# Optimization experiments

Hardware: AMD Instinct MI355X
Metric: run time of the kernel (lower is better)

Reference implementation:

```python
import jax, jax.numpy as jnp
import numpy as np
import math

B, CIN, W = 8, 1, 1024
D, H, NL, NE, DFF = 256, 2, 2, 10, 1024
LAT = W // 2
DK = D // H

def _pe_table(max_len, d):
    pos = np.arange(max_len)[:, None].astype(np.float32)
    div = np.exp(np.arange(0, d, 2).astype(np.float32) * (-math.log(10000.0) / d))
    pe = np.zeros((max_len, d), np.float32)
    pe[:, 0::2] = np.sin(pos * div)
    pe[:, 1::2] = np.cos(pos * div)
    return jnp.asarray(pe[None])

def _ln(x, g, b, eps=1e-5):
    mu = jnp.mean(x, -1, keepdims=True)
    var = jnp.mean(jnp.square(x - mu), -1, keepdims=True)
    return (x - mu) * jax.lax.rsqrt(var + eps) * g + b

def setup_inputs() -> dict:
    key = jax.random.key(0)
    ks = iter(jax.random.split(key, 64))
    tn = lambda shape: 0.02 * jax.random.truncated_normal(next(ks), -2.0, 2.0, shape, jnp.float32)
    return dict(
        x=jax.random.normal(next(ks), (B, CIN, W), jnp.float32),
        conv_w=tn((D, CIN, 5)), conv_b=tn((D,)),
        pe=_pe_table(LAT, D),
        ln0_g=jnp.ones((D,), jnp.float32), ln0_b=jnp.zeros((D,), jnp.float32),
        wq=tn((NL, D, D)), bq=tn((NL, D)),
        wk=tn((NL, D, D)), bk=tn((NL, D)),
        wv=tn((NL, D, D)), bv=tn((NL, D)),
        wo=tn((NL, D, D)), bo=tn((NL, D)),
        ln1_g=jnp.ones((NL, D), jnp.float32), ln1_b=jnp.zeros((NL, D), jnp.float32),
        ln2_g=jnp.ones((NL, D), jnp.float32), ln2_b=jnp.zeros((NL, D), jnp.float32),
        router_w=tn((NL, NE, D)), router_b=tn((NL, NE)),
        e_w1=tn((NL, NE, D, DFF)), e_b1=tn((NL, NE, DFF)),
        e_w2=tn((NL, NE, DFF, D)), e_b2=tn((NL, NE, D)),
        deconv_w=tn((D, D, 4)), deconv_b=tn((D,)),
        lin1_w=tn((128, D)), lin1_b=tn((128,)),
        lin2_w=tn((1, 128)), lin2_b=tn((1,)),
    )

def _forward(x, conv_w, conv_b, pe, ln0_g, ln0_b, wq, bq, wk, bk, wv, bv, wo, bo,
             ln1_g, ln1_b, ln2_g, ln2_b, router_w, router_b,
             e_w1, e_b1, e_w2, e_b2, deconv_w, deconv_b,
             lin1_w, lin1_b, lin2_w, lin2_b):
    # Conv1d(k=5, p=2, replicate) tokenizer + LPPool1d(p=2, k=2, s=2)
    xp = jnp.pad(x, ((0, 0), (0, 0), (2, 2)), mode='edge')
    h = jax.lax.conv_general_dilated(xp, conv_w, window_strides=(1,), padding=[(0, 0)],
                                     dimension_numbers=('NCH', 'OIH', 'NCH'))
    h = h + conv_b[None, :, None]
    h = jnp.sqrt(jnp.sum(jnp.square(h).reshape(B, D, LAT, 2), -1))   # LP pool, p=2
    z = h.transpose(0, 2, 1) + pe                                     # [B, LAT, D]
    z = _ln(z, ln0_g, ln0_b)
    counts_l, rprob_l = [], []
    for l in range(NL):
        q = (z @ wq[l].T + bq[l]).reshape(B, LAT, H, DK).transpose(0, 2, 1, 3)
        k = (z @ wk[l].T + bk[l]).reshape(B, LAT, H, DK).transpose(0, 2, 1, 3)
        v = (z @ wv[l].T + bv[l]).reshape(B, LAT, H, DK).transpose(0, 2, 1, 3)
        attn = jax.nn.softmax(jnp.einsum('bhqd,bhkd->bhqk', q, k) / math.sqrt(DK), -1)
        a = jnp.einsum('bhqk,bhkd->bhqd', attn, v).transpose(0, 2, 1, 3).reshape(B, LAT, D)
        z = _ln(z + (a @ wo[l].T + bo[l]), ln1_g[l], ln1_b[l])
        # Switch FFN: top-1 routing, no token drop, scale output by max route prob
        t = z.reshape(-1, D)                                          # [T, D]
        rp = jax.nn.softmax(t @ router_w[l].T + router_b[l], -1)      # [T, E]
        routes = jnp.argmax(rp, -1)
        rmax = jnp.max(rp, -1)
        hh = jax.nn.relu(jnp.einsum('td,edf->tef', t, e_w1[l]) + e_b1[l])
        yy = jnp.einsum('tef,efd->ted', hh, e_w2[l]) + e_b2[l]
        y = yy[jnp.arange(t.shape[0]), routes] * rmax[:, None]
        counts_l.append(jnp.sum(jax.nn.one_hot(routes, NE, dtype=jnp.float32), 0))
        rprob_l.append(jnp.sum(rp, 0))
        z = _ln(z + y.reshape(B, LAT, D), ln2_g[l], ln2_b[l])
    # ConvTranspose1d(k=4, s=2, p=1) == dilated conv with flipped/transposed kernel
    dw = jnp.flip(deconv_w, -1).transpose(1, 0, 2)                    # [out, in, k]
    u = jax.lax.conv_general_dilated(z.transpose(0, 2, 1), dw, window_strides=(1,),
                                     padding=[(2, 2)], lhs_dilation=(2,),
                                     dimension_numbers=('NCH', 'OIH', 'NCH'))
    u = (u + deconv_b[None, :, None]).transpose(0, 2, 1)              # [B, W, D]
    u = jnp.tanh(u @ lin1_w.T + lin1_b)
    out = (u @ lin2_w.T + lin2_b).transpose(0, 2, 1)                  # [B, 1, W]
    counts = jnp.stack(counts_l)                                      # [NL, NE]
    rprob = jnp.stack(rprob_l)
    total = jnp.sum(counts, -1, keepdims=True)
    loss_moe = NE * jnp.sum((counts / total) * (rprob / total))
    return out, loss_moe

def reference(x, conv_w, conv_b, pe, ln0_g, ln0_b, wq, bq, wk, bk, wv, bv, wo, bo,
              ln1_g, ln1_b, ln2_g, ln2_b, router_w, router_b,
              e_w1, e_b1, e_w2, e_b2, deconv_w, deconv_b,
              lin1_w, lin1_b, lin2_w, lin2_b):
    return _forward(x, conv_w, conv_b, pe, ln0_g, ln0_b, wq, bq, wk, bk, wv, bv, wo, bo,
                    ln1_g, ln1_b, ln2_g, ln2_b, router_w, router_b,
                    e_w1, e_b1, e_w2, e_b2, deconv_w, deconv_b,
                    lin1_w, lin1_b, lin2_w, lin2_b)
```

## Files before the change

kernel.cpp:

```cpp
#include <hip/hip_runtime.h>
#include <math.h>

#define LATN 512
#define DN 256
#define DKN 128
#define TTOT 4096
#define NEXP 10
#define DFFN 1024

using bf16x8 = __attribute__((ext_vector_type(8))) short;
using f32x4  = __attribute__((ext_vector_type(4))) float;

__device__ __forceinline__ float dot4(float4 a, float4 b) {
    return a.x*b.x + a.y*b.y + a.z*b.z + a.w*b.w;
}

__device__ __forceinline__ unsigned short f2bf(float f) {
    union { float f; unsigned int u; } v; v.f = f;
    unsigned int u = v.u + 0x7FFFu + ((v.u >> 16) & 1u);
    return (unsigned short)(u >> 16);
}

__device__ __forceinline__ float block_reduce_sum(float v, float* red) {
    #pragma unroll
    for (int off = 32; off; off >>= 1) v += __shfl_down(v, off, 64);
    int lane = threadIdx.x & 63, wid = threadIdx.x >> 6;
    if (lane == 0) red[wid] = v;
    __syncthreads();
    float r = red[0] + red[1] + red[2] + red[3];
    __syncthreads();
    return r;
}

__device__ __forceinline__ float wave_sum(float x) {
    #pragma unroll
    for (int off = 32; off; off >>= 1) x += __shfl_xor(x, off, 64);
    return x;
}

__global__ void zero_kernel(float* rprob_p, int* ec_p) {
    int i = threadIdx.x;
    if (i < 320) { rprob_p[i] = 0.f; ec_p[i] = 0; }
}

__global__ void tokenizer_kernel(const float* __restrict__ x, const float* __restrict__ cw,
                                 const float* __restrict__ cb, const float* __restrict__ pe,
                                 const float* __restrict__ g, const float* __restrict__ bb,
                                 float* __restrict__ z) {
    int blk = blockIdx.x;
    int l = blk & (LATN - 1);
    int b = blk >> 9;
    int d = threadIdx.x;
    __shared__ float red[8];
    const float* xb = x + (size_t)b * 1024;
    float w0 = cw[d*5+0], w1 = cw[d*5+1], w2 = cw[d*5+2], w3 = cw[d*5+3], w4 = cw[d*5+4];
    float bv = cb[d];
    int p0 = 2 * l;
    auto xc = [&](int i) { return xb[min(max(i, 0), 1023)]; };
    float h0 = bv + w0*xc(p0-2) + w1*xc(p0-1) + w2*xc(p0)   + w3*xc(p0+1) + w4*xc(p0+2);
    float h1 = bv + w0*xc(p0-1) + w1*xc(p0)   + w2*xc(p0+1) + w3*xc(p0+2) + w4*xc(p0+3);
    float pool = sqrtf(h0*h0 + h1*h1);
    float val = pool + pe[l*DN + d];
    float s = block_reduce_sum(val, red);
    float mu = s * (1.0f/DN);
    float dv = val - mu;
    float s2 = block_reduce_sum(dv*dv, red);
    float r = rsqrtf(s2 * (1.0f/DN) + 1e-5f);
    z[((size_t)b*LATN + l)*DN + d] = dv*r*g[d] + bb[d];
}

__global__ void pack_proj(const float* __restrict__ wq, const float* __restrict__ wk,
                          const float* __restrict__ wv, const float* __restrict__ wo,
                          unsigned short* __restrict__ wp) {
    int mat = blockIdx.y;
    int l0 = mat >> 2, which = mat & 3;
    const float* base = (which == 0) ? wq : (which == 1) ? wk : (which == 2) ? wv : wo;
    const float* W = base + l0*65536;
    int tid = blockIdx.x*256 + threadIdx.x;
    int l = tid & 63, kk = (tid >> 6) & 7, nt = tid >> 9;
    const float* src = W + (size_t)(nt*16 + (l&15))*DN + kk*32 + (l>>4)*8;
    unsigned short o[8];
    #pragma unroll
    for (int j = 0; j < 8; ++j) o[j] = f2bf(src[j]);
    *(ulonglong2*)(wp + (size_t)mat*65536 + (size_t)tid*8) = *(ulonglong2*)o;
}

template<int OM>
__device__ __forceinline__ void proj_body(const float* __restrict__ A,
                                          const unsigned short* __restrict__ wpm,
                                          const float* __restrict__ bias,
                                          void* __restrict__ outp, int t0, float oscale,
                                          unsigned short* ts) {
    int tid = threadIdx.x;
    #pragma unroll
    for (int i = 0; i < 16; ++i) {
        int f4 = i*256 + tid;
        int row = f4 >> 6, c4 = f4 & 63;
        float4 a = *(const float4*)&A[(size_t)(t0+row)*DN + c4*4];
        ushort4 o = { f2bf(a.x), f2bf(a.y), f2bf(a.z), f2bf(a.w) };
        *(ushort4*)&ts[row*264 + c4*4] = o;
    }
    __syncthreads();
    int w = tid >> 6, l = tid & 63;
    f32x4 acc[4][4];
    #pragma unroll
    for (int m = 0; m < 4; ++m)
        #pragma unroll
        for (int n = 0; n < 4; ++n) acc[m][n] = (f32x4){0.f,0.f,0.f,0.f};
    const bf16x8* wv = (const bf16x8*)wpm;
    #pragma unroll
    for (int kk = 0; kk < 8; ++kk) {
        bf16x8 af[4];
        #pragma unroll
        for (int m = 0; m < 4; ++m)
            af[m] = *(const bf16x8*)&ts[(m*16 + (l&15))*264 + kk*32 + (l>>4)*8];
        #pragma unroll
        for (int n = 0; n < 4; ++n) {
            bf16x8 bf = wv[((w*4 + n)*8 + kk)*64 + l];
            #pragma unroll
            for (int m = 0; m < 4; ++m)
                acc[m][n] = __builtin_amdgcn_mfma_f32_16x16x32_bf16(af[m], bf, acc[m][n], 0, 0, 0);
        }
    }
    #pragma unroll
    for (int n = 0; n < 4; ++n) {
        int col = w*64 + n*16 + (l&15);
        float bv2 = bias[col];
        #pragma unroll
        for (int m = 0; m < 4; ++m) {
            #pragma unroll
            for (int r = 0; r < 4; ++r) {
                int row = t0 + m*16 + (l>>4)*4 + r;
                float val = acc[m][n][r] + bv2;
                if (OM == 0)
                    ((float*)outp)[(size_t)row*DN + col] = val;
                else if (OM == 1)
                    ((unsigned short*)outp)[(size_t)row*DN + col] = f2bf(val * oscale);
                else
                    ((unsigned short*)outp)[(((size_t)(row>>9)*2 + (col>>7))*128 + (col&127))*512 + (row&511)] = f2bf(val);
            }
        }
    }
}

__global__ __launch_bounds__(256)
void proj_qkv(const float* __restrict__ z, const unsigned short* __restrict__ wp,
              const float* __restrict__ bq, const float* __restrict__ bk,
              const float* __restrict__ bv,
              unsigned short* __restrict__ qb, unsigned short* __restrict__ kb,
              unsigned short* __restrict__ vtb) {
    __shared__ unsigned short ts[64*264];
    int mat = blockIdx.y;
    if (mat == 0)      proj_body<1>(z, wp,          bq, qb,  blockIdx.x*64, 0.08838834764831844f, ts);
    else if (mat == 1) proj_body<1>(z, wp + 65536,  bk, kb,  blockIdx.x*64, 1.0f, ts);
    else               proj_body<2>(z, wp + 131072, bv, vtb, blockIdx.x*64, 1.0f, ts);
}

__global__ __launch_bounds__(256)
void proj_one(const float* __restrict__ A, const unsigned short* __restrict__ wpm,
              const float* __restrict__ bias, float* __restrict__ out) {
    __shared__ unsigned short ts[64*264];
    proj_body<0>(A, wpm, bias, out, blockIdx.x*64, 1.0f, ts);
}

__global__ __launch_bounds__(256)
void attn_mfma(const unsigned short* __restrict__ qb, const unsigned short* __restrict__ kb,
               const unsigned short* __restrict__ vtb, float* __restrict__ a) {
    int blk = blockIdx.x;
    int xcd = blk & 7, idx = blk >> 3;
    int bh = xcd*2 + (idx & 1);
    int qt = idx >> 1;
    int b = bh >> 1, h = bh & 1;
    int q0 = qt * 32;
    int tid = threadIdx.x;
    int w = tid >> 6, l = tid & 63;
    int c = l & 15, g = l >> 4;

    __shared__ __align__(16) unsigned short p_lds[32*512];
    __shared__ float smax[4][2][16];
    __shared__ float ssum[4][2][16];

    bf16x8 qf_[2][4];
    #pragma unroll
    for (int qf = 0; qf < 2; ++qf)
        #pragma unroll
        for (int kk = 0; kk < 4; ++kk)
            qf_[qf][kk] = *(const bf16x8*)&qb[((size_t)(b*LATN + q0 + qf*16 + c))*DN + h*DKN + kk*32 + g*8];

    f32x4 st[8][2];
    #pragma unroll
    for (int f = 0; f < 8; ++f) { st[f][0] = (f32x4){0,0,0,0}; st[f][1] = (f32x4){0,0,0,0}; }
    #pragma unroll
    for (int f = 0; f < 8; ++f) {
        int kbase = w*128 + f*16;
        bf16x8 kf[4];
        #pragma unroll
        for (int kk = 0; kk < 4; ++kk)
            kf[kk] = *(const bf16x8*)&kb[((size_t)(b*LATN + kbase + c))*DN + h*DKN + kk*32 + g*8];
        #pragma unroll
        for (int kk = 0; kk < 4; ++kk) {
            st[f][0] = __builtin_amdgcn_mfma_f32_16x16x32_bf16(kf[kk], qf_[0][kk], st[f][0], 0, 0, 0);
            st[f][1] = __builtin_amdgcn_mfma_f32_16x16x32_bf16(kf[kk], qf_[1][kk], st[f][1], 0, 0, 0);
        }
    }

    float gmax[2], ginv[2];
    #pragma unroll
    for (int qf = 0; qf < 2; ++qf) {
        float m = -1e30f;
        #pragma unroll
        for (int f = 0; f < 8; ++f)
            #pragma unroll
            for (int r = 0; r < 4; ++r) m = fmaxf(m, st[f][qf][r]);
        m = fmaxf(m, __shfl_xor(m, 16, 64));
        m = fmaxf(m, __shfl_xor(m, 32, 64));
        if (l < 16) smax[w][qf][l] = m;
    }
    __syncthreads();
    #pragma unroll
    for (int qf = 0; qf < 2; ++qf)
        gmax[qf] = fmaxf(fmaxf(smax[0][qf][c], smax[1][qf][c]),
                         fmaxf(smax[2][qf][c], smax[3][qf][c]));
    #pragma unroll
    for (int qf = 0; qf < 2; ++qf) {
        float s = 0.f;
        #pragma unroll
        for (int f = 0; f < 8; ++f)
            #pragma unroll
            for (int r = 0; r < 4; ++r) {
                float e = __expf(st[f][qf][r] - gmax[qf]);
                st[f][qf][r] = e; s += e;
            }
        s += __shfl_xor(s, 16, 64);
        s += __shfl_xor(s, 32, 64);
        if (l < 16) ssum[w][qf][l] = s;
    }
    __syncthreads();
    #pragma unroll
    for (int qf = 0; qf < 2; ++qf)
        ginv[qf] = 1.0f / (ssum[0][qf][c] + ssum[1][qf][c] + ssum[2][qf][c] + ssum[3][qf][c]);

    #pragma unroll
    for (int qf = 0; qf < 2; ++qf) {
        int q_ = qf*16 + c;
        int rowb = q_ * 1024;
        int swz = (q_ & 7) << 4;
        float iv = ginv[qf];
        #pragma unroll
        for (int f = 0; f < 8; ++f) {
            unsigned int lo = (unsigned int)f2bf(st[f][qf][0]*iv) |
                              ((unsigned int)f2bf(st[f][qf][1]*iv) << 16);
            unsigned int hi = (unsigned int)f2bf(st[f][qf][2]*iv) |
                              ((unsigned int)f2bf(st[f][qf][3]*iv) << 16);
            int key0 = w*128 + f*16 + g*4;
            *(unsigned long long*)((char*)p_lds + rowb + ((key0*2) ^ swz)) =
                (unsigned long long)lo | ((unsigned long long)hi << 32);
        }
    }
    __syncthreads();

    f32x4 o[2][2];
    o[0][0] = (f32x4){0,0,0,0}; o[0][1] = (f32x4){0,0,0,0};
    o[1][0] = (f32x4){0,0,0,0}; o[1][1] = (f32x4){0,0,0,0};
    #pragma unroll
    for (int kk = 0; kk < 16; ++kk) {
        bf16x8 pb[2];
        #pragma unroll
        for (int qf = 0; qf < 2; ++qf) {
            int q_ = qf*16 + c;
            pb[qf] = *(const bf16x8*)((const char*)p_lds + q_*1024 +
                                      (((kk*32 + g*8)*2) ^ ((q_&7)<<4)));
        }
        bf16x8 va[2];
        #pragma unroll
        for (int m = 0; m < 2; ++m)
            va[m] = *(const bf16x8*)&vtb[((size_t)(bh*128 + w*32 + m*16 + c))*512 + kk*32 + g*8];
        #pragma unroll
        for (int m = 0; m < 2; ++m) {
            o[m][0] = __builtin_amdgcn_mfma_f32_16x16x32_bf16(va[m], pb[0], o[m][0], 0, 0, 0);
            o[m][1] = __builtin_amdgcn_mfma_f32_16x16x32_bf16(va[m], pb[1], o[m][1], 0, 0, 0);
        }
    }
    #pragma unroll
    for (int m = 0; m < 2; ++m)
        #pragma unroll
        for (int qf = 0; qf < 2; ++qf)
            #pragma unroll
            for (int r = 0; r < 4; ++r) {
                int d = w*32 + m*16 + g*4 + r;
                a[((size_t)(b*LATN + q0 + qf*16 + c))*DN + h*DKN + d] = o[m][qf][r];
            }
}

__global__ void ln_residual(float* __restrict__ z, const float* __restrict__ y,
                            const float* __restrict__ g, const float* __restrict__ b) {
    int t = blockIdx.x, tid = threadIdx.x;
    __shared__ float red[8];
    float val = z[(size_t)t*DN + tid] + y[(size_t)t*DN + tid];
    float s = block_reduce_sum(val, red);
    float mu = s * (1.0f/DN);
    float dv = val - mu;
    float s2 = block_reduce_sum(dv*dv, red);
    float r = rsqrtf(s2 * (1.0f/DN) + 1e-5f);
    z[(size_t)t*DN + tid] = dv*r*g[tid] + b[tid];
}

#define RTOK 32
__global__ __launch_bounds__(512)
void router_kernel(const float* __restrict__ z, const float* __restrict__ rw,
                   const float* __restrict__ rb, float* __restrict__ rmaxv,
                   float* __restrict__ rprob_p, int* __restrict__ ec_p,
                   int* __restrict__ elist) {
    __shared__ float rws[NEXP*DN];
    __shared__ float sprob[NEXP];
    __shared__ int lcnt[NEXP], lbase[NEXP];
    __shared__ int lrank[RTOK];
    __shared__ int lam[RTOK];
    int tid = threadIdx.x;
    for (int i = tid; i < NEXP*DN; i += 512) rws[i] = rw[i];
    if (tid < NEXP) { sprob[tid] = 0.f; lcnt[tid] = 0; }
    __syncthreads();
    int g = tid >> 4, j = tid & 15;
    int t = blockIdx.x * RTOK + g;
    const float4* z4 = (const float4*)&z[(size_t)t*DN + j*16];
    const float4* rws4 = (const float4*)rws;
    float acc[NEXP];
    #pragma unroll
    for (int e = 0; e < NEXP; ++e) acc[e] = 0.f;
    int r0 = (j >> 1) & 3;
    #pragma unroll
    for (int kq = 0; kq < 4; ++kq) {
        int k4 = (kq + r0) & 3;
        float4 zv = z4[k4];
        #pragma unroll
        for (int e = 0; e < NEXP; ++e)
            acc[e] += dot4(zv, rws4[e*64 + j*4 + k4]);
    }
    #pragma unroll
    for (int e = 0; e < NEXP; ++e) {
        acc[e] += __shfl_xor(acc[e], 1, 64);
        acc[e] += __shfl_xor(acc[e], 2, 64);
        acc[e] += __shfl_xor(acc[e], 4, 64);
        acc[e] += __shfl_xor(acc[e], 8, 64);
    }
    if (j == 0) {
        float lg[NEXP];
        float m = acc[0] + rb[0]; int am = 0;
        lg[0] = m;
        #pragma unroll
        for (int e = 1; e < NEXP; ++e) {
            lg[e] = acc[e] + rb[e];
            if (lg[e] > m) { m = lg[e]; am = e; }
        }
        float p[NEXP], s = 0.f;
        #pragma unroll
        for (int e = 0; e < NEXP; ++e) { p[e] = expf(lg[e] - m); s += p[e]; }
        float inv = 1.0f / s;
        rmaxv[t] = p[am] * inv;
        lam[g] = am;
        lrank[g] = atomicAdd(&lcnt[am], 1);
        #pragma unroll
        for (int e = 0; e < NEXP; ++e) atomicAdd(&sprob[e], p[e] * inv);
    }
    __syncthreads();
    if (tid < NEXP) {
        lbase[tid] = atomicAdd(&ec_p[tid*16], lcnt[tid]);
        atomicAdd(&rprob_p[tid*16], sprob[tid]);
    }
    __syncthreads();
    if (j == 0)
        elist[lam[g]*TTOT + lbase[lam[g]] + lrank[g]] = t;
}

__global__ void pack_w1(const float* __restrict__ w1l, unsigned short* __restrict__ w1p) {
    int tid = blockIdx.x*256 + threadIdx.x;
    int l = tid & 63, kk = (tid >> 6) & 7, nt = (tid >> 9) & 63, e = tid >> 15;
    const float* src = w1l + (size_t)e*262144 + (size_t)(kk*32 + (l>>4)*8)*DFFN + nt*16 + (l&15);
    unsigned short o[8];
    #pragma unroll
    for (int j = 0; j < 8; ++j) o[j] = f2bf(src[(size_t)j*DFFN]);
    ulonglong2* dst = (ulonglong2*)(w1p + (size_t)tid*8);
    *dst = *(ulonglong2*)o;
}

__global__ void pack_w2(const float* __restrict__ w2l, unsigned short* __restrict__ w2p) {
    int tid = blockIdx.x*256 + threadIdx.x;
    int l = tid & 63, kk = (tid >> 6) & 31, nt = (tid >> 11) & 15, e = tid >> 15;
    const float* src = w2l + (size_t)e*262144 + (size_t)(kk*32 + (l>>4)*8)*DN + nt*16 + (l&15);
    unsigned short o[8];
    #pragma unroll
    for (int j = 0; j < 8; ++j) o[j] = f2bf(src[(size_t)j*DN]);
    ulonglong2* dst = (ulonglong2*)(w2p + (size_t)tid*8);
    *dst = *(ulonglong2*)o;
}

#define TM 16
__global__ __launch_bounds__(256)
void moe_kernel(float* __restrict__ z, const int* __restrict__ elist,
                const int* __restrict__ ec_p, const float* __restrict__ rmaxv,
                const unsigned short* __restrict__ w1p, const float* __restrict__ b1,
                const unsigned short* __restrict__ w2p, const float* __restrict__ b2,
                const float* __restrict__ g, const float* __restrict__ bb) {
    int e = blockIdx.y;
    int cnt = ec_p[e*16];
    int base = blockIdx.x * TM;
    if (base >= cnt) return;
    int n = min(TM, cnt - base);

    __shared__ __align__(16) unsigned short ts[16*264];
    __shared__ __align__(16) unsigned short hbuf[16*1032];
    __shared__ __align__(16) float ybuf[16*260];
    __shared__ int toks[16];
    __shared__ float rm[16];

    int tid = threadIdx.x;
    int w = tid >> 6, l = tid & 63;
    if (tid < 16) {
        int tt = (tid < n) ? elist[e*TTOT + base + tid] : 0;
        toks[tid] = tt;
        rm[tid] = rmaxv[tt];
    }
    __syncthreads();
    #pragma unroll
    for (int m = 0; m < 16; ++m)
        ts[m*264 + tid] = f2bf(z[(size_t)toks[m]*DN + tid]);
    __syncthreads();

    const bf16x8* w1v = (const bf16x8*)w1p;
    const float* b1e = b1 + e*DFFN;
    f32x4 acc[16];
    #pragma unroll
    for (int i = 0; i < 16; ++i) acc[i] = (f32x4){0.f,0.f,0.f,0.f};
    #pragma unroll
    for (int kk = 0; kk < 8; ++kk) {
        bf16x8 a = *(const bf16x8*)(ts + (l&15)*264 + kk*32 + (l>>4)*8);
        const bf16x8* wbp = w1v + (((size_t)e*64 + w*16)*8 + kk)*64 + l;
        #pragma unroll
        for (int nt2 = 0; nt2 < 16; ++nt2)
            acc[nt2] = __builtin_amdgcn_mfma_f32_16x16x32_bf16(a, wbp[nt2*512], acc[nt2], 0, 0, 0);
    }
    #pragma unroll
    for (int nt2 = 0; nt2 < 16; ++nt2) {
        int col = w*256 + nt2*16 + (l&15);
        float bv = b1e[col];
        #pragma unroll
        for (int r = 0; r < 4; ++r) {
            int row = (l>>4)*4 + r;
            hbuf[row*1032 + col] = f2bf(fmaxf(acc[nt2][r] + bv, 0.f));
        }
    }
    __syncthreads();

    const bf16x8* w2v = (const bf16x8*)w2p;
    const float* b2e = b2 + e*DN;
    f32x4 acc2[4];
    #pragma unroll
    for (int i = 0; i < 4; ++i) acc2[i] = (f32x4){0.f,0.f,0.f,0.f};
    for (int kk = 0; kk < 32; ++kk) {
        bf16x8 a = *(const bf16x8*)(hbuf + (l&15)*1032 + kk*32 + (l>>4)*8);
        const bf16x8* wbp = w2v + (((size_t)e*16 + w*4)*32 + kk)*64 + l;
        #pragma unroll
        for (int nt2 = 0; nt2 < 4; ++nt2)
            acc2[nt2] = __builtin_amdgcn_mfma_f32_16x16x32_bf16(a, wbp[nt2*2048], acc2[nt2], 0, 0, 0);
    }
    #pragma unroll
    for (int nt2 = 0; nt2 < 4; ++nt2) {
        int col = w*64 + nt2*16 + (l&15);
        float bv = b2e[col];
        #pragma unroll
        for (int r = 0; r < 4; ++r) {
            int row = (l>>4)*4 + r;
            ybuf[row*260 + col] = (acc2[nt2][r] + bv) * rm[row];
        }
    }
    __syncthreads();

    #pragma unroll
    for (int rr = 0; rr < 4; ++rr) {
        int row = w*4 + rr;
        if (row < n) {
            int t = toks[row];
            float v[4];
            #pragma unroll
            for (int c = 0; c < 4; ++c)
                v[c] = ybuf[row*260 + l + 64*c] + z[(size_t)t*DN + l + 64*c];
            float s = wave_sum(v[0]+v[1]+v[2]+v[3]);
            float mu = s * (1.0f/DN);
            float s2 = 0.f;
            #pragma unroll
            for (int c = 0; c < 4; ++c) { v[c] -= mu; s2 += v[c]*v[c]; }
            s2 = wave_sum(s2);
            float rs = rsqrtf(s2 * (1.0f/DN) + 1e-5f);
            #pragma unroll
            for (int c = 0; c < 4; ++c) {
                int col = l + 64*c;
                z[(size_t)t*DN + col] = v[c]*rs*g[col] + bb[col];
            }
        }
    }
}

__global__ void pack_deconv_mfma(const float* __restrict__ w, unsigned short* __restrict__ wdp) {
    int tid = blockIdx.x*256 + threadIdx.x;
    int l = tid & 63, kk = (tid >> 6) & 7, nt = (tid >> 9) & 15, tap = tid >> 13;
    int dout = nt*16 + (l&15);
    int din0 = kk*32 + (l>>4)*8;
    unsigned short o[8];
    #pragma unroll
    for (int j = 0; j < 8; ++j)
        o[j] = f2bf(w[((size_t)(din0 + j)*DN + dout)*4 + tap]);
    *(ulonglong2*)(wdp + (size_t)tid*8) = *(ulonglong2*)o;
}

__global__ void pack_lin1(const float* __restrict__ w, unsigned short* __restrict__ wl1) {
    int tid = blockIdx.x*256 + threadIdx.x;
    int l = tid & 63, kk = (tid >> 6) & 7, nt = tid >> 9;
    const float* src = w + (size_t)(nt*16 + (l&15))*DN + kk*32 + (l>>4)*8;
    unsigned short o[8];
    #pragma unroll
    for (int j = 0; j < 8; ++j) o[j] = f2bf(src[j]);
    *(ulonglong2*)(wl1 + (size_t)tid*8) = *(ulonglong2*)o;
}

__global__ __launch_bounds__(256)
void deconv_mfma(const float* __restrict__ z, const unsigned short* __restrict__ wdp,
                 const float* __restrict__ db, float* __restrict__ u) {
    int blk = blockIdx.x;
    int b = blk >> 4, lt = blk & 15;
    int l0 = lt * 32;
    __shared__ __align__(16) unsigned short zs[34*264];
    int tid = threadIdx.x;
    #pragma unroll
    for (int i = 0; i < 9; ++i) {
        int f4 = i*256 + tid;
        if (f4 < 34*64) {
            int row = f4 >> 6, c4 = f4 & 63;
            int l = l0 - 1 + row;
            float4 a = (l >= 0 && l < LATN)
                ? *(const float4*)&z[((size_t)b*LATN + l)*DN + c4*4]
                : make_float4(0.f, 0.f, 0.f, 0.f);
            ushort4 o = { f2bf(a.x), f2bf(a.y), f2bf(a.z), f2bf(a.w) };
            *(ushort4*)&zs[row*264 + c4*4] = o;
        }
    }
    __syncthreads();
    int w = tid >> 6, l = tid & 63;
    f32x4 acce[2][4], acco[2][4];
    #pragma unroll
    for (int m = 0; m < 2; ++m)
        #pragma unroll
        for (int n = 0; n < 4; ++n) {
            acce[m][n] = (f32x4){0.f,0.f,0.f,0.f};
            acco[m][n] = (f32x4){0.f,0.f,0.f,0.f};
        }
    const bf16x8* wdv = (const bf16x8*)wdp;
    #pragma unroll
    for (int kk = 0; kk < 8; ++kk) {
        bf16x8 a0[2], a1[2], a2[2];
        #pragma unroll
        for (int m = 0; m < 2; ++m) {
            int rb = (m*16 + (l&15))*264 + kk*32 + (l>>4)*8;
            a0[m] = *(const bf16x8*)&zs[rb];
            a1[m] = *(const bf16x8*)&zs[rb + 264];
            a2[m] = *(const bf16x8*)&zs[rb + 528];
        }
        #pragma unroll
        for (int n = 0; n < 4; ++n) {
            int nt = w*4 + n;
            bf16x8 bt0 = wdv[((0*16 + nt)*8 + kk)*64 + l];
            bf16x8 bt1 = wdv[((1*16 + nt)*8 + kk)*64 + l];
            bf16x8 bt2 = wdv[((2*16 + nt)*8 + kk)*64 + l];
            bf16x8 bt3 = wdv[((3*16 + nt)*8 + kk)*64 + l];
            #pragma unroll
            for (int m = 0; m < 2; ++m) {
                acco[m][n] = __builtin_amdgcn_mfma_f32_16x16x32_bf16(a2[m], bt0, acco[m][n], 0, 0, 0);
                acce[m][n] = __builtin_amdgcn_mfma_f32_16x16x32_bf16(a1[m], bt1, acce[m][n], 0, 0, 0);
                acco[m][n] = __builtin_amdgcn_mfma_f32_16x16x32_bf16(a1[m], bt2, acco[m][n], 0, 0, 0);
                acce[m][n] = __builtin_amdgcn_mfma_f32_16x16x32_bf16(a0[m], bt3, acce[m][n], 0, 0, 0);
            }
        }
    }
    #pragma unroll
    for (int n = 0; n < 4; ++n) {
        int col = (w*4 + n)*16 + (l&15);
        float bv = db[col];
        #pragma unroll
        for (int m = 0; m < 2; ++m) {
            #pragma unroll
            for (int r = 0; r < 4; ++r) {
                int rt = m*16 + (l>>4)*4 + r;
                int wpos = 2*(l0 + rt);
                u[((size_t)b*1024 + wpos)*DN + col]     = acce[m][n][r] + bv;
                u[((size_t)b*1024 + wpos + 1)*DN + col] = acco[m][n][r] + bv;
            }
        }
    }
}

__global__ __launch_bounds__(256)
void head_mfma(const float* __restrict__ u, const unsigned short* __restrict__ wl1,
               const float* __restrict__ b1, const float* __restrict__ w2,
               const float* __restrict__ b2, float* __restrict__ out) {
    int r0 = blockIdx.x * 64;
    __shared__ __align__(16) unsigned short us[64*264];
    __shared__ float part[4][64];
    int tid = threadIdx.x;
    #pragma unroll
    for (int i = 0; i < 16; ++i) {
        int f4 = i*256 + tid;
        int row = f4 >> 6, c4 = f4 & 63;
        float4 a = *(const float4*)&u[(size_t)(r0 + row)*DN + c4*4];
        ushort4 o = { f2bf(a.x), f2bf(a.y), f2bf(a.z), f2bf(a.w) };
        *(ushort4*)&us[row*264 + c4*4] = o;
    }
    __syncthreads();
    int w = tid >> 6, l = tid & 63;
    f32x4 acc[4][2];
    #pragma unroll
    for (int m = 0; m < 4; ++m) { acc[m][0] = (f32x4){0.f,0.f,0.f,0.f}; acc[m][1] = (f32x4){0.f,0.f,0.f,0.f}; }
    const bf16x8* wv1 = (const bf16x8*)wl1;
    #pragma unroll
    for (int kk = 0; kk < 8; ++kk) {
        bf16x8 af[4];
        #pragma unroll
        for (int m = 0; m < 4; ++m)
            af[m] = *(const bf16x8*)&us[(m*16 + (l&15))*264 + kk*32 + (l>>4)*8];
        #pragma unroll
        for (int n = 0; n < 2; ++n) {
            bf16x8 bf = wv1[((w*2 + n)*8 + kk)*64 + l];
            #pragma unroll
            for (int m = 0; m < 4; ++m)
                acc[m][n] = __builtin_amdgcn_mfma_f32_16x16x32_bf16(af[m], bf, acc[m][n], 0, 0, 0);
        }
    }
    float pm[4][4];
    #pragma unroll
    for (int m = 0; m < 4; ++m)
        #pragma unroll
        for (int r = 0; r < 4; ++r) pm[m][r] = 0.f;
    #pragma unroll
    for (int n = 0; n < 2; ++n) {
        int col = (w*2 + n)*16 + (l&15);
        float bb1 = b1[col], ww2 = w2[col];
        #pragma unroll
        for (int m = 0; m < 4; ++m)
            #pragma unroll
            for (int r = 0; r < 4; ++r)
                pm[m][r] += tanhf(acc[m][n][r] + bb1) * ww2;
    }
    #pragma unroll
    for (int off = 1; off <= 8; off <<= 1)
        #pragma unroll
        for (int m = 0; m < 4; ++m)
            #pragma unroll
            for (int r = 0; r < 4; ++r)
                pm[m][r] += __shfl_xor(pm[m][r], off, 64);
    if ((l & 15) == 0) {
        #pragma unroll
        for (int m = 0; m < 4; ++m)
            #pragma unroll
            for (int r = 0; r < 4; ++r)
                part[w][m*16 + (l>>4)*4 + r] = pm[m][r];
    }
    __syncthreads();
    if (tid < 64)
        out[r0 + tid] = part[0][tid] + part[1][tid] + part[2][tid] + part[3][tid] + b2[0];
}

__global__ void loss_kernel(const int* __restrict__ ec_p, const float* __restrict__ rprob_p,
                            float* __restrict__ out) {
    if (threadIdx.x == 0) {
        float s = 0;
        for (int l = 0; l < 2; ++l)
            for (int e = 0; e < NEXP; ++e)
                s += (float)ec_p[l*160 + e*16] * rprob_p[l*160 + e*16];
        out[8192] = 10.0f * s / (4096.0f * 4096.0f);
    }
}

extern "C" void kernel_launch(void* const* d_in, const int* in_sizes, int n_in,
                              void* d_out, int out_size, void* d_ws, size_t ws_size,
                              hipStream_t stream) {
    const float* x        = (const float*)d_in[0];
    const float* conv_w   = (const float*)d_in[1];
    const float* conv_b   = (const float*)d_in[2];
    const float* pe       = (const float*)d_in[3];
    const float* ln0_g    = (const float*)d_in[4];
    const float* ln0_b    = (const float*)d_in[5];
    const float* wq       = (const float*)d_in[6];
    const float* bq       = (const float*)d_in[7];
    const float* wk       = (const float*)d_in[8];
    const float* bk       = (const float*)d_in[9];
    const float* wv       = (const float*)d_in[10];
    const float* bv       = (const float*)d_in[11];
    const float* wo       = (const float*)d_in[12];
    const float* bo       = (const float*)d_in[13];
    const float* ln1_g    = (const float*)d_in[14];
    const float* ln1_b    = (const float*)d_in[15];
    const float* ln2_g    = (const float*)d_in[16];
    const float* ln2_b    = (const float*)d_in[17];
    const float* router_w = (const float*)d_in[18];
    const float* router_b = (const float*)d_in[19];
    const float* e_w1     = (const float*)d_in[20];
    const float* e_b1     = (const float*)d_in[21];
    const float* e_w2     = (const float*)d_in[22];
    const float* e_b2     = (const float*)d_in[23];
    const float* deconv_w = (const float*)d_in[24];
    const float* deconv_b = (const float*)d_in[25];
    const float* lin1_w   = (const float*)d_in[26];
    const float* lin1_b   = (const float*)d_in[27];
    const float* lin2_w   = (const float*)d_in[28];
    const float* lin2_b   = (const float*)d_in[29];

    float* ws = (float*)d_ws;
    const size_t M = 1048576;
    float* z    = ws;
    unsigned short* qb  = (unsigned short*)(ws + 1*M);
    unsigned short* kb  = (unsigned short*)(ws + 2*M);
    unsigned short* vtb = (unsigned short*)(ws + 3*M);
    float* a    = ws + 4*M;
    float* y    = ws + 5*M;
    float* rmax = ws + 6*M;
    float* rprob_p = rmax + 4096;
    int* ec_p   = (int*)(rprob_p + 320);
    int* elist  = ec_p + 320;
    unsigned short* wproj = (unsigned short*)(ws + 6*M + 98304);
    unsigned short* w1p = (unsigned short*)(ws + 1*M);
    unsigned short* w2p = (unsigned short*)(ws + 3*M);
    float* u    = ws + 1*M;
    unsigned short* wdp = (unsigned short*)(ws + 3*M);
    unsigned short* wl1 = (unsigned short*)(ws + 3*M + 131072 + 64);
    float* out  = (float*)d_out;

    zero_kernel<<<1, 512, 0, stream>>>(rprob_p, ec_p);
    {
        dim3 pg(32, 8);
        pack_proj<<<pg, 256, 0, stream>>>(wq, wk, wv, wo, wproj);
    }
    tokenizer_kernel<<<TTOT, 256, 0, stream>>>(x, conv_w, conv_b, pe, ln0_g, ln0_b, z);

    for (int l = 0; l < 2; ++l) {
        const unsigned short* wpl = wproj + (size_t)l*4*65536;
        dim3 qkvg(64, 3);
        proj_qkv<<<qkvg, 256, 0, stream>>>(z, wpl, bq + l*256, bk + l*256, bv + l*256,
                                           qb, kb, vtb);
        attn_mfma<<<256, 256, 0, stream>>>(qb, kb, vtb, a);
        proj_one<<<64, 256, 0, stream>>>(a, wpl + 3*65536, bo + l*256, y);
        ln_residual<<<TTOT, 256, 0, stream>>>(z, y, ln1_g + l*256, ln1_b + l*256);
        router_kernel<<<TTOT/RTOK, 512, 0, stream>>>(z, router_w + l*2560, router_b + l*10,
                                                     rmax, rprob_p + l*160, ec_p + l*160,
                                                     elist + l*10*TTOT);
        pack_w1<<<1280, 256, 0, stream>>>(e_w1 + (size_t)l*2621440, w1p);
        pack_w2<<<1280, 256, 0, stream>>>(e_w2 + (size_t)l*2621440, w2p);
        dim3 mg(TTOT/TM, NEXP);
        moe_kernel<<<mg, 256, 0, stream>>>(z, elist + l*10*TTOT, ec_p + l*160, rmax,
                                           w1p, e_b1 + l*10240,
                                           w2p, e_b2 + l*2560,
                                           ln2_g + l*256, ln2_b + l*256);
    }

    pack_deconv_mfma<<<128, 256, 0, stream>>>(deconv_w, wdp);
    pack_lin1<<<16, 256, 0, stream>>>(lin1_w, wl1);
    deconv_mfma<<<128, 256, 0, stream>>>(z, wdp, deconv_b, u);
    head_mfma<<<128, 256, 0, stream>>>(u, wl1, lin1_b, lin2_w, lin2_b, out);
    loss_kernel<<<1, 64, 0, stream>>>(ec_p, rprob_p, out);
}
```

Before: 272.9 us.

## Restructure MoE kernel: 32-token tiles, chunked FFN hidden, in-register LayerNorm

The MoE expert kernel now handles 32 tokens per block instead of 16, so each weight fragment loaded from global memory feeds two MFMA row tiles. The 1024-wide hidden layer is processed in four 256-column chunks and fed straight into the second GEMM, which shrinks the shared hidden buffer and removes the fp32 output staging buffer. LayerNorm is computed from the MFMA accumulators using shuffle and shared-memory partial sums of x and x². A 1-D grid maps block ids to experts, spreading experts across consecutive blocks. The trade-offs are more synchronisation per block, half as many blocks for load balance, and a single-pass variance formula that is less numerically robust.

```diff
diff --git a/kernel.cpp b/kernel.cpp
--- a/kernel.cpp
+++ b/kernel.cpp
@@ -30,12 +30,6 @@
     float r = red[0] + red[1] + red[2] + red[3];
     __syncthreads();
     return r;
-}
-
-__device__ __forceinline__ float wave_sum(float x) {
-    #pragma unroll
-    for (int off = 32; off; off >>= 1) x += __shfl_xor(x, off, 64);
-    return x;
 }
 
 __global__ void zero_kernel(float* rprob_p, int* ec_p) {
@@ -394,110 +388,162 @@
     *dst = *(ulonglong2*)o;
 }
 
-#define TM 16
+#define TM 32
 __global__ __launch_bounds__(256)
 void moe_kernel(float* __restrict__ z, const int* __restrict__ elist,
                 const int* __restrict__ ec_p, const float* __restrict__ rmaxv,
                 const unsigned short* __restrict__ w1p, const float* __restrict__ b1,
                 const unsigned short* __restrict__ w2p, const float* __restrict__ b2,
                 const float* __restrict__ g, const float* __restrict__ bb) {
-    int e = blockIdx.y;
+    int bid = blockIdx.x;
+    int slot = bid & 15;
+    int e = (slot & 7) + 8*(slot >> 3);
+    if (e >= NEXP) return;
+    int tile = bid >> 4;
     int cnt = ec_p[e*16];
-    int base = blockIdx.x * TM;
+    int base = tile * TM;
     if (base >= cnt) return;
     int n = min(TM, cnt - base);
 
-    __shared__ __align__(16) unsigned short ts[16*264];
-    __shared__ __align__(16) unsigned short hbuf[16*1032];
-    __shared__ __align__(16) float ybuf[16*260];
-    __shared__ int toks[16];
-    __shared__ float rm[16];
+    __shared__ __align__(16) unsigned short ts[32*264];
+    __shared__ __align__(16) unsigned short hch[32*264];
+    __shared__ float wsum[4][32], wsq[4][32];
+    __shared__ int toks[32];
+    __shared__ float rm[32];
 
     int tid = threadIdx.x;
-    int w = tid >> 6, l = tid & 63;
-    if (tid < 16) {
+    int w = tid >> 6, l = tid & 63, c = l & 15, gq = l >> 4;
+    if (tid < 32) {
         int tt = (tid < n) ? elist[e*TTOT + base + tid] : 0;
         toks[tid] = tt;
         rm[tid] = rmaxv[tt];
     }
     __syncthreads();
     #pragma unroll
-    for (int m = 0; m < 16; ++m)
+    for (int m = 0; m < 32; ++m)
         ts[m*264 + tid] = f2bf(z[(size_t)toks[m]*DN + tid]);
     __syncthreads();
 
     const bf16x8* w1v = (const bf16x8*)w1p;
+    const bf16x8* w2v = (const bf16x8*)w2p;
     const float* b1e = b1 + e*DFFN;
-    f32x4 acc[16];
-    #pragma unroll
-    for (int i = 0; i < 16; ++i) acc[i] = (f32x4){0.f,0.f,0.f,0.f};
-    #pragma unroll
-    for (int kk = 0; kk < 8; ++kk) {
-        bf16x8 a = *(const bf16x8*)(ts + (l&15)*264 + kk*32 + (l>>4)*8);
-        const bf16x8* wbp = w1v + (((size_t)e*64 + w*16)*8 + kk)*64 + l;
-        #pragma unroll
-        for (int nt2 = 0; nt2 < 16; ++nt2)
-            acc[nt2] = __builtin_amdgcn_mfma_f32_16x16x32_bf16(a, wbp[nt2*512], acc[nt2], 0, 0, 0);
-    }
-    #pragma unroll
-    for (int nt2 = 0; nt2 < 16; ++nt2) {
-        int col = w*256 + nt2*16 + (l&15);
-        float bv = b1e[col];
+    f32x4 acc2[2][4];
+    #pragma unroll
+    for (int m = 0; m < 2; ++m)
+        #pragma unroll
+        for (int nn = 0; nn < 4; ++nn) acc2[m][nn] = (f32x4){0.f,0.f,0.f,0.f};
+
+    for (int fc = 0; fc < 4; ++fc) {
+        f32x4 acc1[2][4];
+        #pragma unroll
+        for (int m = 0; m < 2; ++m)
+            #pragma unroll
+            for (int nn = 0; nn < 4; ++nn) acc1[m][nn] = (f32x4){0.f,0.f,0.f,0.f};
+        #pragma unroll
+        for (int kk = 0; kk < 8; ++kk) {
+            bf16x8 af[2];
+            #pragma unroll
+            for (int m = 0; m < 2; ++m)
+                af[m] = *(const bf16x8*)&ts[(m*16 + c)*264 + kk*32 + gq*8];
+            #pragma unroll
+            for (int nn = 0; nn < 4; ++nn) {
+                int ntg = fc*16 + w*4 + nn;
+                bf16x8 bf = w1v[(((size_t)e*64 + ntg)*8 + kk)*64 + l];
+                #pragma unroll
+                for (int m = 0; m < 2; ++m)
+                    acc1[m][nn] = __builtin_amdgcn_mfma_f32_16x16x32_bf16(af[m], bf, acc1[m][nn], 0, 0, 0);
+            }
+        }
+        #pragma unroll
+        for (int nn = 0; nn < 4; ++nn) {
+            int col = w*64 + nn*16 + c;
+            float bv = b1e[fc*256 + col];
+            #pragma unroll
+            for (int m = 0; m < 2; ++m)
+                #pragma unroll
+                for (int r = 0; r < 4; ++r) {
+                    int row = m*16 + gq*4 + r;
+                    hch[row*264 + col] = f2bf(fmaxf(acc1[m][nn][r] + bv, 0.f));
+                }
+        }
+        __syncthreads();
+        #pragma unroll
+        for (int kk = 0; kk < 8; ++kk) {
+            bf16x8 hf[2];
+            #pragma unroll
+            for (int m = 0; m < 2; ++m)
+                hf[m] = *(const bf16x8*)&hch[(m*16 + c)*264 + kk*32 + gq*8];
+            #pragma unroll
+            for (int nn = 0; nn < 4; ++nn) {
+                bf16x8 bf = w2v[(((size_t)e*16 + w*4 + nn)*32 + fc*8 + kk)*64 + l];
+                #pragma unroll
+                for (int m = 0; m < 2; ++m)
+                    acc2[m][nn] = __builtin_amdgcn_mfma_f32_16x16x32_bf16(hf[m], bf, acc2[m][nn], 0, 0, 0);
+            }
+        }
+        __syncthreads();
+    }
+
+    const float* b2e = b2 + e*DN;
+    float vals[2][4][4];
+    float sm[2][4], sq[2][4];
+    #pragma unroll
+    for (int m = 0; m < 2; ++m)
+        #pragma unroll
+        for (int r = 0; r < 4; ++r) { sm[m][r] = 0.f; sq[m][r] = 0.f; }
+    #pragma unroll
+    for (int m = 0; m < 2; ++m)
+        #pragma unroll
+        for (int nn = 0; nn < 4; ++nn) {
+            int colg = w*64 + nn*16 + c;
+            float bv = b2e[colg];
+            #pragma unroll
+            for (int r = 0; r < 4; ++r) {
+                int row = m*16 + gq*4 + r;
+                float v = (acc2[m][nn][r] + bv) * rm[row] + z[(size_t)toks[row]*DN + colg];
+                vals[m][nn][r] = v;
+                sm[m][r] += v; sq[m][r] += v*v;
+            }
+        }
+    #pragma unroll
+    for (int m = 0; m < 2; ++m)
         #pragma unroll
         for (int r = 0; r < 4; ++r) {
-            int row = (l>>4)*4 + r;
-            hbuf[row*1032 + col] = f2bf(fmaxf(acc[nt2][r] + bv, 0.f));
-        }
-    }
-    __syncthreads();
-
-    const bf16x8* w2v = (const bf16x8*)w2p;
-    const float* b2e = b2 + e*DN;
-    f32x4 acc2[4];
-    #pragma unroll
-    for (int i = 0; i < 4; ++i) acc2[i] = (f32x4){0.f,0.f,0.f,0.f};
-    for (int kk = 0; kk < 32; ++kk) {
-        bf16x8 a = *(const bf16x8*)(hbuf + (l&15)*1032 + kk*32 + (l>>4)*8);
-        const bf16x8* wbp = w2v + (((size_t)e*16 + w*4)*32 + kk)*64 + l;
-        #pragma unroll
-        for (int nt2 = 0; nt2 < 4; ++nt2)
-            acc2[nt2] = __builtin_amdgcn_mfma_f32_16x16x32_bf16(a, wbp[nt2*2048], acc2[nt2], 0, 0, 0);
-    }
-    #pragma unroll
-    for (int nt2 = 0; nt2 < 4; ++nt2) {
-        int col = w*64 + nt2*16 + (l&15);
-        float bv = b2e[col];
+            #pragma unroll
+            for (int off = 1; off <= 8; off <<= 1) {
+                sm[m][r] += __shfl_xor(sm[m][r], off, 64);
+                sq[m][r] += __shfl_xor(sq[m][r], off, 64);
+            }
+        }
+    if (c == 0) {
+        #pragma unroll
+        for (int m = 0; m < 2; ++m)
+            #pragma unroll
+            for (int r = 0; r < 4; ++r) {
+                wsum[w][m*16 + gq*4 + r] = sm[m][r];
+                wsq[w][m*16 + gq*4 + r] = sq[m][r];
+            }
+    }
+    __syncthreads();
+    #pragma unroll
+    for (int m = 0; m < 2; ++m)
         #pragma unroll
         for (int r = 0; r < 4; ++r) {
-            int row = (l>>4)*4 + r;
-            ybuf[row*260 + col] = (acc2[nt2][r] + bv) * rm[row];
-        }
-    }
-    __syncthreads();
-
-    #pragma unroll
-    for (int rr = 0; rr < 4; ++rr) {
-        int row = w*4 + rr;
-        if (row < n) {
-            int t = toks[row];
-            float v[4];
-            #pragma unroll
-            for (int c = 0; c < 4; ++c)
-                v[c] = ybuf[row*260 + l + 64*c] + z[(size_t)t*DN + l + 64*c];
-            float s = wave_sum(v[0]+v[1]+v[2]+v[3]);
-            float mu = s * (1.0f/DN);
-            float s2 = 0.f;
-            #pragma unroll
-            for (int c = 0; c < 4; ++c) { v[c] -= mu; s2 += v[c]*v[c]; }
-            s2 = wave_sum(s2);
-            float rs = rsqrtf(s2 * (1.0f/DN) + 1e-5f);
-            #pragma unroll
-            for (int c = 0; c < 4; ++c) {
-                int col = l + 64*c;
-                z[(size_t)t*DN + col] = v[c]*rs*g[col] + bb[col];
-            }
-        }
-    }
+            int row = m*16 + gq*4 + r;
+            float S = wsum[0][row] + wsum[1][row] + wsum[2][row] + wsum[3][row];
+            float Q = wsq[0][row] + wsq[1][row] + wsq[2][row] + wsq[3][row];
+            float mu = S * (1.0f/DN);
+            float var = Q * (1.0f/DN) - mu*mu;
+            float rs = rsqrtf(var + 1e-5f);
+            if (row < n) {
+                int t = toks[row];
+                #pragma unroll
+                for (int nn = 0; nn < 4; ++nn) {
+                    int colg = w*64 + nn*16 + c;
+                    z[(size_t)t*DN + colg] = (vals[m][nn][r] - mu)*rs*g[colg] + bb[colg];
+                }
+            }
+        }
 }
 
 __global__ void pack_deconv_mfma(const float* __restrict__ w, unsigned short* __restrict__ wdp) {
@@ -752,11 +798,10 @@
                                                      elist + l*10*TTOT);
         pack_w1<<<1280, 256, 0, stream>>>(e_w1 + (size_t)l*2621440, w1p);
         pack_w2<<<1280, 256, 0, stream>>>(e_w2 + (size_t)l*2621440, w2p);
-        dim3 mg(TTOT/TM, NEXP);
-        moe_kernel<<<mg, 256, 0, stream>>>(z, elist + l*10*TTOT, ec_p + l*160, rmax,
-                                           w1p, e_b1 + l*10240,
-                                           w2p, e_b2 + l*2560,
-                                           ln2_g + l*256, ln2_b + l*256);
+        moe_kernel<<<2048, 256, 0, stream>>>(z, elist + l*10*TTOT, ec_p + l*160, rmax,
+                                             w1p, e_b1 + l*10240,
+                                             w2p, e_b2 + l*2560,
+                                             ln2_g + l*256, ln2_b + l*256);
     }
 
     pack_deconv_mfma<<<128, 256, 0, stream>>>(deconv_w, wdp);
```

Measured after the change: 436.0 us. 1.6x slower.
